# Optimization experiments

Hardware: AMD Instinct MI355X
Metric: run time of the kernel (lower is better)

The kernel has to match this reference:

```python
import jax, jax.numpy as jnp
import numpy as np

B, S, D = 8, 2048, 256


def setup_inputs() -> dict:
    key = jax.random.key(0)
    k1, k2, k3, k4, k5 = jax.random.split(key, 5)
    head = jax.random.normal(k1, (B, S, D), dtype=jnp.float32)
    dep = jax.random.normal(k2, (B, S, D), dtype=jnp.float32)
    edge_U = jax.random.normal(k3, (D, D), dtype=jnp.float32) / np.sqrt(D)
    edge_W = jax.random.normal(k4, (1, 2 * D), dtype=jnp.float32) / np.sqrt(2 * D)
    edge_b = jax.random.normal(k5, (1,), dtype=jnp.float32)
    return {"head": head, "dep": dep, "edge_U": edge_U, "edge_W": edge_W, "edge_b": edge_b}


def reference(head, dep, edge_U, edge_W, edge_b):
    # t1[b,i,o] = head[b,i,:] @ U @ dep[b,o,:]  -> [B,S,S]
    t1 = jnp.einsum('bid,de,boe->bio', head, edge_U, dep)
    # t2: linear over pairwise concat(head_i, dep_o); decomposes into two
    # broadcast-added matvecs (same math as W @ concat, no [B,S^2,2D] tensor).
    d = head.shape[-1]
    wh, wd = edge_W[0, :d], edge_W[0, d:]
    hs = head @ wh  # [B,S]
    ds = dep @ wd   # [B,S]
    t2 = hs[:, :, None] + ds[:, None, :]  # [B,S,S]
    return t1 + t2 + edge_b[0]
```

## Files before the change

kernel.cpp:

```cpp
#include <hip/hip_runtime.h>
#include <hip/hip_bf16.h>
#include <stdint.h>
#include <stddef.h>

#define B_ 8
#define S_ 2048
#define D_ 256
#define NROWS (B_ * S_)

typedef __attribute__((ext_vector_type(8))) short short8;
typedef __attribute__((ext_vector_type(4))) short short4v;
typedef __attribute__((ext_vector_type(4))) float f32x4;

__device__ __forceinline__ short bf16of(float f) {
  union { float f; unsigned u; } x; x.f = f;
  unsigned r = x.u + 0x7FFFu + ((x.u >> 16) & 1u);
  return (short)(r >> 16);
}

__device__ __forceinline__ void async_ld16(const void* g, void* s) {
  __builtin_amdgcn_global_load_lds(
      (const __attribute__((address_space(1))) void*)g,
      (__attribute__((address_space(3))) void*)s, 16, 0, 0);
}

__device__ __forceinline__ void stage_tile(const short* __restrict__ g_row0,
                                           char* lds_base, int t, int kk0) {
#pragma unroll
  for (int c = 0; c < 4; ++c) {
    int p = c * 256 + t;
    int r = p >> 3;
    int sl = (p & 7) ^ (r & 7);
    async_ld16(g_row0 + (size_t)r * D_ + kk0 + sl * 8, lds_base + p * 16);
  }
}

__global__ void k_prep_u(const float* __restrict__ U, short* __restrict__ UT) {
  int n = blockIdx.x;
  int k = threadIdx.x;
  UT[n * D_ + k] = bf16of(U[k * D_ + n]);
}

__global__ void k_rows(const float* __restrict__ head, const float* __restrict__ dep,
                       const float* __restrict__ W,
                       float* __restrict__ hs, float* __restrict__ ds,
                       short* __restrict__ headB, short* __restrict__ depB) {
  const float* X; const float* wv; float* sv; short* XB;
  if (blockIdx.y == 0) { X = head; wv = W;      sv = hs; XB = headB; }
  else                 { X = dep;  wv = W + D_; sv = ds; XB = depB;  }
  const int row = blockIdx.x * 4 + (threadIdx.x >> 6);
  const int l = threadIdx.x & 63;
  const float4 v  = *(const float4*)(X + (size_t)row * D_ + l * 4);
  const float4 wq = *(const float4*)(wv + l * 4);
  short4v pk;
  pk[0] = bf16of(v.x); pk[1] = bf16of(v.y); pk[2] = bf16of(v.z); pk[3] = bf16of(v.w);
  *(short4v*)(XB + (size_t)row * D_ + l * 4) = pk;
  float p = v.x * wq.x + v.y * wq.y + v.z * wq.z + v.w * wq.w;
  p += __shfl_xor(p, 1); p += __shfl_xor(p, 2); p += __shfl_xor(p, 4);
  p += __shfl_xor(p, 8); p += __shfl_xor(p, 16); p += __shfl_xor(p, 32);
  if (l == 0) sv[row] = p;
}

__launch_bounds__(256, 2)
__global__ void k_ahat(const short* __restrict__ headB, const short* __restrict__ UT,
                       short* __restrict__ Ahat) {
  __shared__ __align__(16) short sU[2 * 128 * 64];
  __shared__ __align__(16) short sH[2 * 128 * 64];
  const int t = threadIdx.x;
  const int w = t >> 6;
  const int l = t & 63;
  const int quad = l >> 4;
  const int r15 = l & 15;
  const int sw = r15 & 7;
  const int nbase = blockIdx.x * 128;
  const int mbase = blockIdx.y * 128;

  const short* gA = UT + (size_t)nbase * D_;
  const short* gB = headB + (size_t)mbase * D_;

  f32x4 acc[4][4];
#pragma unroll
  for (int i = 0; i < 4; ++i)
#pragma unroll
    for (int j = 0; j < 4; ++j) acc[i][j] = (f32x4)0.0f;

  stage_tile(gA, (char*)sU, t, 0);
  stage_tile(gB, (char*)sH, t, 0);
  stage_tile(gA, (char*)sU + 16384, t, 64);
  stage_tile(gB, (char*)sH + 16384, t, 64);

  const int baseA = ((w >> 1) * 64 + r15) * 8;
  const int baseB = ((w & 1) * 64 + r15) * 8;

#pragma unroll
  for (int it = 0; it < 4; ++it) {
    if (it < 3) asm volatile("s_waitcnt vmcnt(8)" ::: "memory");
    else        asm volatile("s_waitcnt vmcnt(0)" ::: "memory");
    __builtin_amdgcn_s_barrier();

    const short8* pA = (const short8*)(sU + (size_t)(it & 1) * (128 * 64));
    const short8* pB = (const short8*)(sH + (size_t)(it & 1) * (128 * 64));
#pragma unroll
    for (int kb = 0; kb < 2; ++kb) {
      const int so = (kb * 4 + quad) ^ sw;
      short8 aF[4], bF[4];
#pragma unroll
      for (int mt = 0; mt < 4; ++mt) aF[mt] = pA[baseA + mt * 128 + so];
#pragma unroll
      for (int nt = 0; nt < 4; ++nt) bF[nt] = pB[baseB + nt * 128 + so];
#pragma unroll
      for (int mt = 0; mt < 4; ++mt)
#pragma unroll
        for (int nt = 0; nt < 4; ++nt)
          acc[mt][nt] = __builtin_amdgcn_mfma_f32_16x16x32_bf16(aF[mt], bF[nt], acc[mt][nt], 0, 0, 0);
    }
    __builtin_amdgcn_s_barrier();
    if (it < 2) {
      stage_tile(gA, (char*)sU + (size_t)(it & 1) * 16384, t, (it + 2) * 64);
      stage_tile(gB, (char*)sH + (size_t)(it & 1) * 16384, t, (it + 2) * 64);
    }
  }

#pragma unroll
  for (int mt = 0; mt < 4; ++mt) {
    int n_loc = (w >> 1) * 64 + mt * 16 + quad * 4;
#pragma unroll
    for (int nt = 0; nt < 4; ++nt) {
      int i_loc = (w & 1) * 64 + nt * 16 + r15;
      short4v pk;
      pk[0] = bf16of(acc[mt][nt][0]); pk[1] = bf16of(acc[mt][nt][1]);
      pk[2] = bf16of(acc[mt][nt][2]); pk[3] = bf16of(acc[mt][nt][3]);
      *(short4v*)(Ahat + (size_t)(mbase + i_loc) * D_ + nbase + n_loc) = pk;
    }
  }
}

__launch_bounds__(256, 2)
__global__ void k_main(const short* __restrict__ Ahat, const short* __restrict__ depB,
                       const float* __restrict__ hs, const float* __restrict__ ds,
                       const float* __restrict__ eb, float* __restrict__ out) {
  __shared__ __align__(16) short sD[2 * 128 * 64];
  __shared__ __align__(16) short sAh[2 * 128 * 64];
  const int t = threadIdx.x;
  const int w = t >> 6;
  const int l = t & 63;
  const int quad = l >> 4;
  const int r15 = l & 15;
  const int sw = r15 & 7;
  const int b = blockIdx.z;
  const int mbase = blockIdx.y * 128;
  const int nbase = blockIdx.x * 128;

  const short* gA = depB + (size_t)(b * S_ + nbase) * D_;
  const short* gB = Ahat + (size_t)(b * S_ + mbase) * D_;

  f32x4 acc[4][4];
#pragma unroll
  for (int i = 0; i < 4; ++i)
#pragma unroll
    for (int j = 0; j < 4; ++j) acc[i][j] = (f32x4)0.0f;

  stage_tile(gA, (char*)sD, t, 0);
  stage_tile(gB, (char*)sAh, t, 0);
  stage_tile(gA, (char*)sD + 16384, t, 64);
  stage_tile(gB, (char*)sAh + 16384, t, 64);

  const int baseA = ((w >> 1) * 64 + r15) * 8;
  const int baseB = ((w & 1) * 64 + r15) * 8;

#pragma unroll
  for (int it = 0; it < 4; ++it) {
    if (it < 3) asm volatile("s_waitcnt vmcnt(8)" ::: "memory");
    else        asm volatile("s_waitcnt vmcnt(0)" ::: "memory");
    __builtin_amdgcn_s_barrier();

    const short8* pA = (const short8*)(sD + (size_t)(it & 1) * (128 * 64));
    const short8* pB = (const short8*)(sAh + (size_t)(it & 1) * (128 * 64));
#pragma unroll
    for (int kb = 0; kb < 2; ++kb) {
      const int so = (kb * 4 + quad) ^ sw;
      short8 aF[4], bF[4];
#pragma unroll
      for (int mt = 0; mt < 4; ++mt) aF[mt] = pA[baseA + mt * 128 + so];
#pragma unroll
      for (int nt = 0; nt < 4; ++nt) bF[nt] = pB[baseB + nt * 128 + so];
#pragma unroll
      for (int mt = 0; mt < 4; ++mt)
#pragma unroll
        for (int nt = 0; nt < 4; ++nt)
          acc[mt][nt] = __builtin_amdgcn_mfma_f32_16x16x32_bf16(aF[mt], bF[nt], acc[mt][nt], 0, 0, 0);
    }
    __builtin_amdgcn_s_barrier();
    if (it < 2) {
      stage_tile(gA, (char*)sD + (size_t)(it & 1) * 16384, t, (it + 2) * 64);
      stage_tile(gB, (char*)sAh + (size_t)(it & 1) * 16384, t, (it + 2) * 64);
    }
  }

  const float bias = eb[0];
  float hv4[4];
#pragma unroll
  for (int nt = 0; nt < 4; ++nt)
    hv4[nt] = hs[(size_t)b * S_ + mbase + (w & 1) * 64 + nt * 16 + r15] + bias;

#pragma unroll
  for (int mt = 0; mt < 4; ++mt) {
    int o_loc = (w >> 1) * 64 + mt * 16 + quad * 4;
    float4 dsv = *(const float4*)(ds + (size_t)b * S_ + nbase + o_loc);
#pragma unroll
    for (int nt = 0; nt < 4; ++nt) {
      int i_loc = (w & 1) * 64 + nt * 16 + r15;
      float hv = hv4[nt];
      f32x4 a = acc[mt][nt];
      float4 o4;
      o4.x = a[0] + hv + dsv.x;
      o4.y = a[1] + hv + dsv.y;
      o4.z = a[2] + hv + dsv.z;
      o4.w = a[3] + hv + dsv.w;
      *(float4*)(out + (size_t)(b * S_ + mbase + i_loc) * S_ + nbase + o_loc) = o4;
    }
  }
}

extern "C" void kernel_launch(void* const* d_in, const int* in_sizes, int n_in,
                              void* d_out, int out_size, void* d_ws, size_t ws_size,
                              hipStream_t stream) {
  const float* head = (const float*)d_in[0];
  const float* dep  = (const float*)d_in[1];
  const float* U    = (const float*)d_in[2];
  const float* W    = (const float*)d_in[3];
  const float* eb   = (const float*)d_in[4];
  float* out = (float*)d_out;

  char* ws = (char*)d_ws;
  short* UT    = (short*)ws;
  float* hs    = (float*)(ws + (128 << 10));
  float* ds    = (float*)(ws + (192 << 10));
  short* headB = (short*)(ws + (256 << 10));
  short* depB  = (short*)(ws + (256 << 10) + (8 << 20));
  short* Ahat  = (short*)(ws + (256 << 10) + (16 << 20));

  k_prep_u<<<dim3(256), dim3(256), 0, stream>>>(U, UT);
  k_rows<<<dim3(NROWS / 4, 2), dim3(256), 0, stream>>>(head, dep, W, hs, ds, headB, depB);
  k_ahat<<<dim3(2, 128), dim3(256), 0, stream>>>(headB, UT, Ahat);
  k_main<<<dim3(16, 16, 8), dim3(256), 0, stream>>>(Ahat, depB, hs, ds, eb, out);
}
```

Measured before the change: 194.0 us.

## Shrink k_main LDS K-tile for higher occupancy, retile k_ahat, use nontemporal stores

k_main now stages 32-wide K slices instead of 64-wide, halving its LDS footprint and raising launch bounds to 4 blocks per CU, with an 8-step double-buffered loop and a new swizzle. k_ahat keeps a full 64x256 slice of U resident in LDS, uses 64-column tiles and launches twice as many blocks. The output stores in k_main become nontemporal so the 128MB streaming output bypasses cache retention. Costs are more barriers per K in k_main and a larger up-front U load in k_ahat.

```diff
diff --git a/kernel.cpp b/kernel.cpp
--- a/kernel.cpp
+++ b/kernel.cpp
@@ -24,13 +24,24 @@
       (__attribute__((address_space(3))) void*)s, 16, 0, 0);
 }
 
-__device__ __forceinline__ void stage_tile(const short* __restrict__ g_row0,
-                                           char* lds_base, int t, int kk0) {
+__device__ __forceinline__ void stage_tile64(const short* __restrict__ g_row0,
+                                             char* lds_base, int t, int kk0) {
 #pragma unroll
   for (int c = 0; c < 4; ++c) {
     int p = c * 256 + t;
     int r = p >> 3;
     int sl = (p & 7) ^ (r & 7);
+    async_ld16(g_row0 + (size_t)r * D_ + kk0 + sl * 8, lds_base + p * 16);
+  }
+}
+
+__device__ __forceinline__ void stage_tile32(const short* __restrict__ g_row0,
+                                             char* lds_base, int t, int kk0) {
+#pragma unroll
+  for (int c = 0; c < 2; ++c) {
+    int p = c * 256 + t;
+    int r = p >> 2;
+    int sl = (p & 3) ^ ((r >> 1) & 3);
     async_ld16(g_row0 + (size_t)r * D_ + kk0 + sl * 8, lds_base + p * 16);
   }
 }
@@ -64,7 +75,7 @@
 __launch_bounds__(256, 2)
 __global__ void k_ahat(const short* __restrict__ headB, const short* __restrict__ UT,
                        short* __restrict__ Ahat) {
-  __shared__ __align__(16) short sU[2 * 128 * 64];
+  __shared__ __align__(16) short sU[64 * 256];
   __shared__ __align__(16) short sH[2 * 128 * 64];
   const int t = threadIdx.x;
   const int w = t >> 6;
@@ -72,81 +83,83 @@
   const int quad = l >> 4;
   const int r15 = l & 15;
   const int sw = r15 & 7;
-  const int nbase = blockIdx.x * 128;
+  const int nbase = blockIdx.x * 64;
   const int mbase = blockIdx.y * 128;
 
-  const short* gA = UT + (size_t)nbase * D_;
+#pragma unroll
+  for (int c = 0; c < 8; ++c) {
+    int p = c * 256 + t;
+    int r = p >> 5;
+    int sl = (p & 31) ^ (r & 7);
+    async_ld16(UT + (size_t)(nbase + r) * D_ + sl * 8, (char*)sU + p * 16);
+  }
   const short* gB = headB + (size_t)mbase * D_;
-
-  f32x4 acc[4][4];
+  stage_tile64(gB, (char*)sH, t, 0);
+  stage_tile64(gB, (char*)sH + 16384, t, 64);
+
+  f32x4 acc[4][2];
 #pragma unroll
   for (int i = 0; i < 4; ++i)
 #pragma unroll
-    for (int j = 0; j < 4; ++j) acc[i][j] = (f32x4)0.0f;
-
-  stage_tile(gA, (char*)sU, t, 0);
-  stage_tile(gB, (char*)sH, t, 0);
-  stage_tile(gA, (char*)sU + 16384, t, 64);
-  stage_tile(gB, (char*)sH + 16384, t, 64);
-
-  const int baseA = ((w >> 1) * 64 + r15) * 8;
-  const int baseB = ((w & 1) * 64 + r15) * 8;
+    for (int j = 0; j < 2; ++j) acc[i][j] = (f32x4)0.0f;
+
+  const int baseB = (w * 32 + r15) * 8;
 
 #pragma unroll
   for (int it = 0; it < 4; ++it) {
-    if (it < 3) asm volatile("s_waitcnt vmcnt(8)" ::: "memory");
+    if (it < 3) asm volatile("s_waitcnt vmcnt(4)" ::: "memory");
     else        asm volatile("s_waitcnt vmcnt(0)" ::: "memory");
     __builtin_amdgcn_s_barrier();
 
-    const short8* pA = (const short8*)(sU + (size_t)(it & 1) * (128 * 64));
+    const short8* pU = (const short8*)sU;
     const short8* pB = (const short8*)(sH + (size_t)(it & 1) * (128 * 64));
 #pragma unroll
     for (int kb = 0; kb < 2; ++kb) {
+      const int slg = it * 8 + kb * 4 + quad;
+      short8 aF[4], bF[2];
+#pragma unroll
+      for (int ar = 0; ar < 4; ++ar)
+        aF[ar] = pU[(ar * 16 + r15) * 32 + (slg ^ sw)];
       const int so = (kb * 4 + quad) ^ sw;
-      short8 aF[4], bF[4];
-#pragma unroll
-      for (int mt = 0; mt < 4; ++mt) aF[mt] = pA[baseA + mt * 128 + so];
-#pragma unroll
-      for (int nt = 0; nt < 4; ++nt) bF[nt] = pB[baseB + nt * 128 + so];
-#pragma unroll
-      for (int mt = 0; mt < 4; ++mt)
-#pragma unroll
-        for (int nt = 0; nt < 4; ++nt)
-          acc[mt][nt] = __builtin_amdgcn_mfma_f32_16x16x32_bf16(aF[mt], bF[nt], acc[mt][nt], 0, 0, 0);
-    }
-    __builtin_amdgcn_s_barrier();
-    if (it < 2) {
-      stage_tile(gA, (char*)sU + (size_t)(it & 1) * 16384, t, (it + 2) * 64);
-      stage_tile(gB, (char*)sH + (size_t)(it & 1) * 16384, t, (it + 2) * 64);
-    }
-  }
-
-#pragma unroll
-  for (int mt = 0; mt < 4; ++mt) {
-    int n_loc = (w >> 1) * 64 + mt * 16 + quad * 4;
-#pragma unroll
-    for (int nt = 0; nt < 4; ++nt) {
-      int i_loc = (w & 1) * 64 + nt * 16 + r15;
+#pragma unroll
+      for (int br = 0; br < 2; ++br)
+        bF[br] = pB[baseB + br * 128 + so];
+#pragma unroll
+      for (int ar = 0; ar < 4; ++ar)
+#pragma unroll
+        for (int br = 0; br < 2; ++br)
+          acc[ar][br] = __builtin_amdgcn_mfma_f32_16x16x32_bf16(aF[ar], bF[br], acc[ar][br], 0, 0, 0);
+    }
+    __builtin_amdgcn_s_barrier();
+    if (it < 2)
+      stage_tile64(gB, (char*)sH + (size_t)(it & 1) * 16384, t, (it + 2) * 64);
+  }
+
+#pragma unroll
+  for (int ar = 0; ar < 4; ++ar) {
+    int n_loc = ar * 16 + quad * 4;
+#pragma unroll
+    for (int br = 0; br < 2; ++br) {
+      int i_loc = w * 32 + br * 16 + r15;
       short4v pk;
-      pk[0] = bf16of(acc[mt][nt][0]); pk[1] = bf16of(acc[mt][nt][1]);
-      pk[2] = bf16of(acc[mt][nt][2]); pk[3] = bf16of(acc[mt][nt][3]);
+      pk[0] = bf16of(acc[ar][br][0]); pk[1] = bf16of(acc[ar][br][1]);
+      pk[2] = bf16of(acc[ar][br][2]); pk[3] = bf16of(acc[ar][br][3]);
       *(short4v*)(Ahat + (size_t)(mbase + i_loc) * D_ + nbase + n_loc) = pk;
     }
   }
 }
 
-__launch_bounds__(256, 2)
+__launch_bounds__(256, 4)
 __global__ void k_main(const short* __restrict__ Ahat, const short* __restrict__ depB,
                        const float* __restrict__ hs, const float* __restrict__ ds,
                        const float* __restrict__ eb, float* __restrict__ out) {
-  __shared__ __align__(16) short sD[2 * 128 * 64];
-  __shared__ __align__(16) short sAh[2 * 128 * 64];
+  __shared__ __align__(16) short sD[2 * 128 * 32];
+  __shared__ __align__(16) short sAh[2 * 128 * 32];
   const int t = threadIdx.x;
   const int w = t >> 6;
   const int l = t & 63;
   const int quad = l >> 4;
   const int r15 = l & 15;
-  const int sw = r15 & 7;
   const int b = blockIdx.z;
   const int mbase = blockIdx.y * 128;
   const int nbase = blockIdx.x * 128;
@@ -160,40 +173,37 @@
 #pragma unroll
     for (int j = 0; j < 4; ++j) acc[i][j] = (f32x4)0.0f;
 
-  stage_tile(gA, (char*)sD, t, 0);
-  stage_tile(gB, (char*)sAh, t, 0);
-  stage_tile(gA, (char*)sD + 16384, t, 64);
-  stage_tile(gB, (char*)sAh + 16384, t, 64);
-
-  const int baseA = ((w >> 1) * 64 + r15) * 8;
-  const int baseB = ((w & 1) * 64 + r15) * 8;
-
-#pragma unroll
-  for (int it = 0; it < 4; ++it) {
-    if (it < 3) asm volatile("s_waitcnt vmcnt(8)" ::: "memory");
+  stage_tile32(gA, (char*)sD, t, 0);
+  stage_tile32(gB, (char*)sAh, t, 0);
+  stage_tile32(gA, (char*)sD + 8192, t, 32);
+  stage_tile32(gB, (char*)sAh + 8192, t, 32);
+
+  const int baseA = ((w >> 1) * 64 + r15) * 4;
+  const int baseB = ((w & 1) * 64 + r15) * 4;
+  const int so = quad ^ ((r15 >> 1) & 3);
+
+#pragma unroll
+  for (int it = 0; it < 8; ++it) {
+    if (it < 7) asm volatile("s_waitcnt vmcnt(4)" ::: "memory");
     else        asm volatile("s_waitcnt vmcnt(0)" ::: "memory");
     __builtin_amdgcn_s_barrier();
 
-    const short8* pA = (const short8*)(sD + (size_t)(it & 1) * (128 * 64));
-    const short8* pB = (const short8*)(sAh + (size_t)(it & 1) * (128 * 64));
-#pragma unroll
-    for (int kb = 0; kb < 2; ++kb) {
-      const int so = (kb * 4 + quad) ^ sw;
-      short8 aF[4], bF[4];
-#pragma unroll
-      for (int mt = 0; mt < 4; ++mt) aF[mt] = pA[baseA + mt * 128 + so];
-#pragma unroll
-      for (int nt = 0; nt < 4; ++nt) bF[nt] = pB[baseB + nt * 128 + so];
-#pragma unroll
-      for (int mt = 0; mt < 4; ++mt)
-#pragma unroll
-        for (int nt = 0; nt < 4; ++nt)
-          acc[mt][nt] = __builtin_amdgcn_mfma_f32_16x16x32_bf16(aF[mt], bF[nt], acc[mt][nt], 0, 0, 0);
-    }
-    __builtin_amdgcn_s_barrier();
-    if (it < 2) {
-      stage_tile(gA, (char*)sD + (size_t)(it & 1) * 16384, t, (it + 2) * 64);
-      stage_tile(gB, (char*)sAh + (size_t)(it & 1) * 16384, t, (it + 2) * 64);
+    const short8* pA = (const short8*)(sD + (size_t)(it & 1) * (128 * 32));
+    const short8* pB = (const short8*)(sAh + (size_t)(it & 1) * (128 * 32));
+    short8 aF[4], bF[4];
+#pragma unroll
+    for (int mt = 0; mt < 4; ++mt) aF[mt] = pA[baseA + mt * 64 + so];
+#pragma unroll
+    for (int nt = 0; nt < 4; ++nt) bF[nt] = pB[baseB + nt * 64 + so];
+#pragma unroll
+    for (int mt = 0; mt < 4; ++mt)
+#pragma unroll
+      for (int nt = 0; nt < 4; ++nt)
+        acc[mt][nt] = __builtin_amdgcn_mfma_f32_16x16x32_bf16(aF[mt], bF[nt], acc[mt][nt], 0, 0, 0);
+    __builtin_amdgcn_s_barrier();
+    if (it < 6) {
+      stage_tile32(gA, (char*)sD + (size_t)(it & 1) * 8192, t, (it + 2) * 32);
+      stage_tile32(gB, (char*)sAh + (size_t)(it & 1) * 8192, t, (it + 2) * 32);
     }
   }
 
@@ -206,18 +216,19 @@
 #pragma unroll
   for (int mt = 0; mt < 4; ++mt) {
     int o_loc = (w >> 1) * 64 + mt * 16 + quad * 4;
-    float4 dsv = *(const float4*)(ds + (size_t)b * S_ + nbase + o_loc);
+    f32x4 dsv = *(const f32x4*)(ds + (size_t)b * S_ + nbase + o_loc);
 #pragma unroll
     for (int nt = 0; nt < 4; ++nt) {
       int i_loc = (w & 1) * 64 + nt * 16 + r15;
       float hv = hv4[nt];
       f32x4 a = acc[mt][nt];
-      float4 o4;
-      o4.x = a[0] + hv + dsv.x;
-      o4.y = a[1] + hv + dsv.y;
-      o4.z = a[2] + hv + dsv.z;
-      o4.w = a[3] + hv + dsv.w;
-      *(float4*)(out + (size_t)(b * S_ + mbase + i_loc) * S_ + nbase + o_loc) = o4;
+      f32x4 o4;
+      o4[0] = a[0] + hv + dsv[0];
+      o4[1] = a[1] + hv + dsv[1];
+      o4[2] = a[2] + hv + dsv[2];
+      o4[3] = a[3] + hv + dsv[3];
+      __builtin_nontemporal_store(o4,
+          (f32x4*)(out + (size_t)(b * S_ + mbase + i_loc) * S_ + nbase + o_loc));
     }
   }
 }
@@ -242,6 +253,6 @@
 
   k_prep_u<<<dim3(256), dim3(256), 0, stream>>>(U, UT);
   k_rows<<<dim3(NROWS / 4, 2), dim3(256), 0, stream>>>(head, dep, W, hs, ds, headB, depB);
-  k_ahat<<<dim3(2, 128), dim3(256), 0, stream>>>(headB, UT, Ahat);
+  k_ahat<<<dim3(4, 128), dim3(256), 0, stream>>>(headB, UT, Ahat);
   k_main<<<dim3(16, 16, 8), dim3(256), 0, stream>>>(Ahat, depB, hs, ds, eb, out);
 }
```

After: 214.8 us. 1.11x slower.
